# Kernel optimization log

Measured on AMD Instinct MI355X. Metric: run time of the kernel, lower is better.

Reference implementation:

```python
import jax, jax.numpy as jnp
import numpy as np


def _conv1x1(x, W, b):
    # x: [b,c,h,w], W: [out,in], b: [out]
    return jnp.einsum('oi,bihw->bohw', W, x) + b[None, :, None, None]


def setup_inputs() -> dict:
    key = jax.random.key(0)
    ks = jax.random.split(key, 8)
    B, C, H, W = 4, 256, 64, 64
    s = 1.0 / np.sqrt(C)
    return {
        'x1': jax.random.normal(ks[0], (B, C, H, W), jnp.float32),
        'x2': jax.random.normal(ks[1], (B, C, H, W), jnp.float32),
        'Wq': jax.random.normal(ks[2], (C, C), jnp.float32) * s,
        'bq': jax.random.normal(ks[3], (C,), jnp.float32) * 0.01,
        'Wk': jax.random.normal(ks[4], (C, C), jnp.float32) * s,
        'bk': jax.random.normal(ks[5], (C,), jnp.float32) * 0.01,
        'Wv': jax.random.normal(ks[6], (C, C), jnp.float32) * s,
        'bv': jax.random.normal(ks[7], (C,), jnp.float32) * 0.01,
    }


def reference(x1, x2, Wq, bq, Wk, bk, Wv, bv):
    b, c, h, w = x1.shape
    n = h * w
    q = _conv1x1(x1, Wq, bq).reshape(b, c, n)   # [b,c,n]
    k = _conv1x1(x2, Wk, bk).reshape(b, c, n)   # [b,c,n]
    v = _conv1x1(x2, Wv, bv).reshape(b, c, n)   # [b,c,n]
    # scores[b,i,j] = sum_c q[b,c,i] * k[b,c,j]; softmax over j (last dim)
    scores = jnp.einsum('bci,bcj->bij', q, k)
    attn = jax.nn.softmax(scores, axis=-1)      # [b,n,n]
    # out[b,c,i] = sum_j v[b,c,j] * attn[b,i,j]  (v @ attn^T)
    out = jnp.einsum('bcj,bij->bci', v, attn)
    return out.reshape(b, c, h, w)
```

## Files before the change

### kernel.cpp

```cpp
#include <hip/hip_runtime.h>

#define BATCH 4
#define CDIM 256
#define NDIM 4096

typedef unsigned short u16;
typedef unsigned int u32;
typedef _Float16 f16;
typedef __attribute__((ext_vector_type(8))) _Float16 half8;
typedef __attribute__((ext_vector_type(4))) float floatx4;

__device__ __forceinline__ void load_lds_128(const void* g, void* l) {
  __builtin_amdgcn_global_load_lds(
      (const __attribute__((address_space(1))) u32*)g,
      (__attribute__((address_space(3))) u32*)l, 16, 0, 0);
}

__global__ __launch_bounds__(256) void prep_w_k(
    const float* __restrict__ wq, const float* __restrict__ wk,
    const float* __restrict__ wv, f16* __restrict__ whq,
    f16* __restrict__ whk, f16* __restrict__ whv) {
  const int gid = blockIdx.x * 256 + threadIdx.x;
  const int a = gid >> 13;
  const int r = gid & 8191;
  const float* src = (a == 0) ? wq : ((a == 1) ? wk : wv);
  f16* dst = (a == 0) ? whq : ((a == 1) ? whk : whv);
  float4 v0 = *(const float4*)(src + r * 8);
  float4 v1 = *(const float4*)(src + r * 8 + 4);
  half8 h;
  h[0] = (f16)v0.x; h[1] = (f16)v0.y; h[2] = (f16)v0.z; h[3] = (f16)v0.w;
  h[4] = (f16)v1.x; h[5] = (f16)v1.y; h[6] = (f16)v1.z; h[7] = (f16)v1.w;
  *(half8*)(dst + r * 8) = h;
}

__global__ __launch_bounds__(256) void transpose_k(
    const float* __restrict__ x1, const float* __restrict__ x2,
    f16* __restrict__ xt1, f16* __restrict__ xt2) {
  __shared__ __align__(16) float tile[64 * 68];
  const int z = blockIdx.z;
  const float* src = (z & 1) ? x2 : x1;
  f16* dst = (z & 1) ? xt2 : xt1;
  const int b = z >> 1;
  src += (size_t)b * CDIM * NDIM;
  dst += (size_t)b * NDIM * CDIM;
  const int n0 = blockIdx.x * 64, c0 = blockIdx.y * 64;
  const int t = threadIdx.x;
#pragma unroll
  for (int it = 0; it < 4; ++it) {
    int chunk = t + it * 256;
    int row = chunk >> 4;
    int col4 = (chunk & 15) << 2;
    float4 v = *(const float4*)(src + (size_t)(c0 + row) * NDIM + (n0 + col4));
    *(float4*)&tile[row * 68 + col4] = v;
  }
  __syncthreads();
#pragma unroll
  for (int it = 0; it < 2; ++it) {
    int task = t + it * 256;
    int nl = task >> 3;
    int cb = (task & 7) << 3;
    half8 h;
#pragma unroll
    for (int j = 0; j < 8; ++j) h[j] = (f16)tile[(cb + j) * 68 + nl];
    *(half8*)(dst + (size_t)(n0 + nl) * CDIM + (c0 + cb)) = h;
  }
}

__global__ __launch_bounds__(256, 2) void proj_qk_k(
    const f16* __restrict__ xt1, const f16* __restrict__ xt2,
    const f16* __restrict__ whq, const float* __restrict__ bq,
    const f16* __restrict__ whk, const float* __restrict__ bk,
    f16* __restrict__ qt, f16* __restrict__ kt) {
  const int z = blockIdx.z;
  const int which = z & 1, b = z >> 1;
  const f16* xt = which ? xt2 : xt1;
  const f16* w = which ? whk : whq;
  const float* bias = which ? bk : bq;
  f16* outp = which ? kt : qt;
  xt += (size_t)b * NDIM * CDIM;
  outp += (size_t)b * NDIM * CDIM;
  const int c0 = blockIdx.x * 128, i0 = blockIdx.y * 128;
  const int tid = threadIdx.x;
  const int wave = tid >> 6, lane = tid & 63, l16 = lane & 15, grp = lane >> 4;
  const int wi = (wave & 1) * 64, wc = (wave >> 1) * 64;
  floatx4 acc[4][4];
#pragma unroll
  for (int mb = 0; mb < 4; ++mb)
#pragma unroll
    for (int nb = 0; nb < 4; ++nb) acc[mb][nb] = (floatx4){0.f, 0.f, 0.f, 0.f};
#pragma unroll
  for (int ks = 0; ks < 8; ++ks) {
    const int kofs = ks * 32 + grp * 8;
    half8 a[4], bb[4];
#pragma unroll
    for (int mb = 0; mb < 4; ++mb)
      a[mb] = *(const half8*)(xt + (size_t)(i0 + wi + mb * 16 + l16) * CDIM + kofs);
#pragma unroll
    for (int nb = 0; nb < 4; ++nb)
      bb[nb] = *(const half8*)(w + (size_t)(c0 + wc + nb * 16 + l16) * CDIM + kofs);
#pragma unroll
    for (int mb = 0; mb < 4; ++mb)
#pragma unroll
      for (int nb = 0; nb < 4; ++nb)
        acc[mb][nb] = __builtin_amdgcn_mfma_f32_16x16x32_f16(a[mb], bb[nb], acc[mb][nb], 0, 0, 0);
  }
#pragma unroll
  for (int nb = 0; nb < 4; ++nb) {
    const int c = c0 + wc + nb * 16 + l16;
    const float bv = bias[c];
#pragma unroll
    for (int mb = 0; mb < 4; ++mb) {
      const int ibase = i0 + wi + mb * 16 + grp * 4;
#pragma unroll
      for (int r = 0; r < 4; ++r)
        outp[(size_t)(ibase + r) * CDIM + c] = (f16)(acc[mb][nb][r] + bv);
    }
  }
}

__global__ __launch_bounds__(256, 2) void proj_v_k(
    const f16* __restrict__ xt2, const f16* __restrict__ whv,
    const float* __restrict__ bv, f16* __restrict__ vsout) {
  const int b = blockIdx.z;
  const f16* xt = xt2 + (size_t)b * NDIM * CDIM;
  f16* outp = vsout + (size_t)b * CDIM * NDIM;
  const int c0 = blockIdx.x * 128, j0 = blockIdx.y * 128;
  const int tid = threadIdx.x;
  const int wave = tid >> 6, lane = tid & 63, l16 = lane & 15, grp = lane >> 4;
  const int wc = (wave & 1) * 64, wj = (wave >> 1) * 64;
  floatx4 acc[4][4];
#pragma unroll
  for (int mb = 0; mb < 4; ++mb)
#pragma unroll
    for (int nb = 0; nb < 4; ++nb) acc[mb][nb] = (floatx4){0.f, 0.f, 0.f, 0.f};
#pragma unroll
  for (int ks = 0; ks < 8; ++ks) {
    const int kofs = ks * 32 + grp * 8;
    half8 a[4], bb[4];
#pragma unroll
    for (int mb = 0; mb < 4; ++mb)
      a[mb] = *(const half8*)(whv + (size_t)(c0 + wc + mb * 16 + l16) * CDIM + kofs);
#pragma unroll
    for (int nb = 0; nb < 4; ++nb)
      bb[nb] = *(const half8*)(xt + (size_t)(j0 + wj + nb * 16 + l16) * CDIM + kofs);
#pragma unroll
    for (int mb = 0; mb < 4; ++mb)
#pragma unroll
      for (int nb = 0; nb < 4; ++nb)
        acc[mb][nb] = __builtin_amdgcn_mfma_f32_16x16x32_f16(a[mb], bb[nb], acc[mb][nb], 0, 0, 0);
  }
#pragma unroll
  for (int mb = 0; mb < 4; ++mb)
#pragma unroll
    for (int r = 0; r < 4; ++r) {
      const int c = c0 + wc + mb * 16 + grp * 4 + r;
      const float bvv = bv[c];
#pragma unroll
      for (int nb = 0; nb < 4; ++nb) {
        const int j = j0 + wj + nb * 16 + l16;
        outp[(size_t)c * NDIM + j] = (f16)(acc[mb][nb][r] + bvv);
      }
    }
}

__global__ __launch_bounds__(256) void flash_k(
    const f16* __restrict__ qt, const f16* __restrict__ kt,
    const f16* __restrict__ vs, float* __restrict__ outp) {
  __shared__ __align__(16) u16 smem[2 * 32768 + 4096];
  const int bx = blockIdx.x;
  const int b = (bx & 7) >> 1;
  const int i0 = ((bx >> 3) + ((bx & 1) << 5)) * 64;
  const f16* Q = qt + (size_t)b * NDIM * CDIM;
  const f16* K = kt + (size_t)b * NDIM * CDIM;
  const f16* V = vs + (size_t)b * CDIM * NDIM;
  float* outg = outp + (size_t)b * CDIM * NDIM;
  const int tid = threadIdx.x;
  const int wave = tid >> 6, lane = tid & 63, l16 = lane & 15, grp = lane >> 4;

  half8 qf[8];
#pragma unroll
  for (int ks = 0; ks < 8; ++ks)
    qf[ks] = *(const half8*)(Q + (size_t)(i0 + wave * 16 + l16) * CDIM + ks * 32 + grp * 8);

  floatx4 O[16];
#pragma unroll
  for (int cb = 0; cb < 16; ++cb) O[cb] = (floatx4){0.f, 0.f, 0.f, 0.f};
  float mrow[4], lrow[4];
#pragma unroll
  for (int r = 0; r < 4; ++r) { mrow[r] = -1e30f; lrow[r] = 0.f; }

  f16* sPh = (f16*)(smem + 65536);
  f16* sPw = sPh + wave * (16 * 64);

  const int kr2 = lane >> 5, kp = lane & 31;
  const int vr = lane >> 3, vp = lane & 7;

#define STAGE(J0, BUF)                                                        \
  {                                                                           \
    u16* bK = (BUF);                                                          \
    u16* bV = (BUF) + 16384;                                                  \
    _Pragma("unroll") for (int it = 0; it < 8; ++it) {                        \
      const int row = wave * 16 + it * 2 + kr2;                               \
      const int g = kp ^ (row & 7);                                           \
      load_lds_128(K + (size_t)((J0) + row) * CDIM + g * 8,                   \
                   &bK[(wave * 16 + it * 2) * 256]);                          \
    }                                                                         \
    _Pragma("unroll") for (int it = 0; it < 8; ++it) {                        \
      const int c = wave * 64 + it * 8 + vr;                                  \
      const int g = vp ^ (c & 7);                                             \
      load_lds_128(V + (size_t)c * NDIM + (J0) + g * 8,                       \
                   &bV[(wave * 64 + it * 8) * 64]);                           \
    }                                                                         \
  }

  STAGE(0, smem)

  for (int t = 0; t < NDIM / 64; ++t) {
    __syncthreads();
    if (t + 1 < NDIM / 64) STAGE((t + 1) * 64, smem + ((t + 1) & 1) * 32768)
    u16* bK = smem + (t & 1) * 32768;
    u16* bV = bK + 16384;

    floatx4 S4[4];
#pragma unroll
    for (int jb = 0; jb < 4; ++jb) S4[jb] = (floatx4){0.f, 0.f, 0.f, 0.f};
#pragma unroll
    for (int ks = 0; ks < 8; ++ks) {
      const int chunk = ks * 4 + grp;
#pragma unroll
      for (int jb = 0; jb < 4; ++jb) {
        const int row = jb * 16 + l16;
        half8 kf = *(const half8*)&bK[row * 256 + ((chunk ^ (row & 7)) << 3)];
        S4[jb] = __builtin_amdgcn_mfma_f32_16x16x32_f16(qf[ks], kf, S4[jb], 0, 0, 0);
      }
    }

    float mnew[4];
#pragma unroll
    for (int r = 0; r < 4; ++r)
      mnew[r] = fmaxf(fmaxf(S4[0][r], S4[1][r]), fmaxf(S4[2][r], S4[3][r]));
#pragma unroll
    for (int mask = 1; mask < 16; mask <<= 1)
#pragma unroll
      for (int r = 0; r < 4; ++r)
        mnew[r] = fmaxf(mnew[r], __shfl_xor(mnew[r], mask, 64));
    float alpha[4];
#pragma unroll
    for (int r = 0; r < 4; ++r) {
      const float mt = fmaxf(mrow[r], mnew[r]);
      alpha[r] = __expf(mrow[r] - mt);
      mrow[r] = mt;
    }
    float rsum[4];
#pragma unroll
    for (int r = 0; r < 4; ++r) {
#pragma unroll
      for (int jb = 0; jb < 4; ++jb) S4[jb][r] = __expf(S4[jb][r] - mrow[r]);
      rsum[r] = (S4[0][r] + S4[1][r]) + (S4[2][r] + S4[3][r]);
    }
#pragma unroll
    for (int mask = 1; mask < 16; mask <<= 1)
#pragma unroll
      for (int r = 0; r < 4; ++r)
        rsum[r] += __shfl_xor(rsum[r], mask, 64);
#pragma unroll
    for (int r = 0; r < 4; ++r) lrow[r] = lrow[r] * alpha[r] + rsum[r];
#pragma unroll
    for (int cb = 0; cb < 16; ++cb)
#pragma unroll
      for (int r = 0; r < 4; ++r) O[cb][r] *= alpha[r];

#pragma unroll
    for (int jb = 0; jb < 4; ++jb)
#pragma unroll
      for (int r = 0; r < 4; ++r) {
        const int row = grp * 4 + r;
        const int col = jb * 16 + l16;
        sPw[row * 64 + (((col >> 3) ^ (row & 7)) << 3) + (col & 7)] = (f16)S4[jb][r];
      }
    half8 pa[2];
#pragma unroll
    for (int ks = 0; ks < 2; ++ks) {
      const int chunk = ks * 4 + grp;
      pa[ks] = *(const half8*)&sPw[l16 * 64 + ((chunk ^ (l16 & 7)) << 3)];
    }

#pragma unroll
    for (int ks = 0; ks < 2; ++ks) {
      const int chunk = ks * 4 + grp;
#pragma unroll
      for (int cb = 0; cb < 16; ++cb) {
        const int c = cb * 16 + l16;
        half8 vf = *(const half8*)&bV[c * 64 + ((chunk ^ (c & 7)) << 3)];
        O[cb] = __builtin_amdgcn_mfma_f32_16x16x32_f16(pa[ks], vf, O[cb], 0, 0, 0);
      }
    }
  }
  __syncthreads();

  float inv[4];
#pragma unroll
  for (int r = 0; r < 4; ++r) inv[r] = 1.0f / lrow[r];
  float* sO = (float*)smem;
#pragma unroll
  for (int cb = 0; cb < 16; ++cb) {
    const int c = cb * 16 + l16;
#pragma unroll
    for (int r = 0; r < 4; ++r)
      sO[c * 68 + wave * 16 + grp * 4 + r] = O[cb][r] * inv[r];
  }
  __syncthreads();
#pragma unroll
  for (int it = 0; it < 16; ++it) {
    const int idx = tid + it * 256;
    const int c = idx >> 4, p = idx & 15;
    float4 v = *(const float4*)&sO[c * 68 + p * 4];
    *(float4*)(outg + (size_t)c * NDIM + i0 + p * 4) = v;
  }
}

extern "C" void kernel_launch(void* const* d_in, const int* in_sizes, int n_in,
                              void* d_out, int out_size, void* d_ws, size_t ws_size,
                              hipStream_t stream) {
  const float* x1 = (const float*)d_in[0];
  const float* x2 = (const float*)d_in[1];
  const float* Wq = (const float*)d_in[2];
  const float* bq = (const float*)d_in[3];
  const float* Wk = (const float*)d_in[4];
  const float* bk = (const float*)d_in[5];
  const float* Wv = (const float*)d_in[6];
  const float* bv = (const float*)d_in[7];
  float* out = (float*)d_out;
  char* ws = (char*)d_ws;
  const size_t SZ = (size_t)BATCH * NDIM * CDIM * sizeof(f16);
  f16* xt1 = (f16*)(ws + 0 * SZ);
  f16* xt2 = (f16*)(ws + 1 * SZ);
  f16* qt  = (f16*)(ws + 2 * SZ);
  f16* kt  = (f16*)(ws + 3 * SZ);
  f16* vsp = (f16*)(ws + 4 * SZ);
  f16* whq = (f16*)(ws + 5 * SZ);
  f16* whk = whq + CDIM * CDIM;
  f16* whv = whk + CDIM * CDIM;

  prep_w_k<<<dim3(96), dim3(256), 0, stream>>>(Wq, Wk, Wv, whq, whk, whv);
  transpose_k<<<dim3(NDIM / 64, CDIM / 64, 2 * BATCH), dim3(256), 0, stream>>>(x1, x2, xt1, xt2);
  proj_qk_k<<<dim3(2, 32, 2 * BATCH), dim3(256), 0, stream>>>(xt1, xt2, whq, bq, whk, bk, qt, kt);
  proj_v_k<<<dim3(2, 32, BATCH), dim3(256), 0, stream>>>(xt2, whv, bv, vsp);
  flash_k<<<dim3(256), dim3(256), 0, stream>>>(qt, kt, vsp, out);
}
```

Before: 290.5 us.

## Split flash attention over key dimension with partial outputs and combine kernel

```diff
diff --git a/kernel.cpp b/kernel.cpp
--- a/kernel.cpp
+++ b/kernel.cpp
@@ -3,6 +3,10 @@
 #define BATCH 4
 #define CDIM 256
 #define NDIM 4096
+#define SPLITS 4
+#define KSPLIT (NDIM / SPLITS)
+#define JT 64
+#define NTILES (KSPLIT / JT)
 
 typedef unsigned short u16;
 typedef unsigned int u32;
@@ -163,67 +167,68 @@
     }
 }
 
-__global__ __launch_bounds__(256) void flash_k(
+__global__ __launch_bounds__(256, 2) void flash_k(
     const f16* __restrict__ qt, const f16* __restrict__ kt,
-    const f16* __restrict__ vs, float* __restrict__ outp) {
-  __shared__ __align__(16) u16 smem[2 * 32768 + 4096];
+    const f16* __restrict__ vs, f16* __restrict__ pO,
+    float* __restrict__ pm, float* __restrict__ pl) {
+  __shared__ __align__(16) u16 smem[32768];
   const int bx = blockIdx.x;
-  const int b = (bx & 7) >> 1;
-  const int i0 = ((bx >> 3) + ((bx & 1) << 5)) * 64;
+  const int c16 = bx & 15;
+  const int b = c16 >> 2, s = c16 & 3;
+  const int i0 = (bx >> 4) * 128;
+  const int jwin = s * KSPLIT;
   const f16* Q = qt + (size_t)b * NDIM * CDIM;
   const f16* K = kt + (size_t)b * NDIM * CDIM;
   const f16* V = vs + (size_t)b * CDIM * NDIM;
-  float* outg = outp + (size_t)b * CDIM * NDIM;
   const int tid = threadIdx.x;
   const int wave = tid >> 6, lane = tid & 63, l16 = lane & 15, grp = lane >> 4;
-
-  half8 qf[8];
-#pragma unroll
-  for (int ks = 0; ks < 8; ++ks)
-    qf[ks] = *(const half8*)(Q + (size_t)(i0 + wave * 16 + l16) * CDIM + ks * 32 + grp * 8);
-
-  floatx4 O[16];
-#pragma unroll
-  for (int cb = 0; cb < 16; ++cb) O[cb] = (floatx4){0.f, 0.f, 0.f, 0.f};
-  float mrow[4], lrow[4];
-#pragma unroll
-  for (int r = 0; r < 4; ++r) { mrow[r] = -1e30f; lrow[r] = 0.f; }
-
-  f16* sPh = (f16*)(smem + 65536);
-  f16* sPw = sPh + wave * (16 * 64);
+  u16* bK = smem;
+  u16* bV = smem + 16384;
+
+  half8 qf[2][8];
+#pragma unroll
+  for (int mb = 0; mb < 2; ++mb)
+#pragma unroll
+    for (int ks = 0; ks < 8; ++ks)
+      qf[mb][ks] = *(const half8*)(Q + (size_t)(i0 + wave * 32 + mb * 16 + l16) * CDIM +
+                                   ks * 32 + grp * 8);
+
+  floatx4 O[2][16];
+#pragma unroll
+  for (int mb = 0; mb < 2; ++mb)
+#pragma unroll
+    for (int cb = 0; cb < 16; ++cb) O[mb][cb] = (floatx4){0.f, 0.f, 0.f, 0.f};
+  float m_[2][4], l_[2][4];
+#pragma unroll
+  for (int mb = 0; mb < 2; ++mb)
+#pragma unroll
+    for (int r = 0; r < 4; ++r) { m_[mb][r] = -1e30f; l_[mb][r] = 0.f; }
 
   const int kr2 = lane >> 5, kp = lane & 31;
   const int vr = lane >> 3, vp = lane & 7;
 
-#define STAGE(J0, BUF)                                                        \
-  {                                                                           \
-    u16* bK = (BUF);                                                          \
-    u16* bV = (BUF) + 16384;                                                  \
-    _Pragma("unroll") for (int it = 0; it < 8; ++it) {                        \
-      const int row = wave * 16 + it * 2 + kr2;                               \
-      const int g = kp ^ (row & 7);                                           \
-      load_lds_128(K + (size_t)((J0) + row) * CDIM + g * 8,                   \
-                   &bK[(wave * 16 + it * 2) * 256]);                          \
-    }                                                                         \
-    _Pragma("unroll") for (int it = 0; it < 8; ++it) {                        \
-      const int c = wave * 64 + it * 8 + vr;                                  \
-      const int g = vp ^ (c & 7);                                             \
-      load_lds_128(V + (size_t)c * NDIM + (J0) + g * 8,                       \
-                   &bV[(wave * 64 + it * 8) * 64]);                           \
-    }                                                                         \
-  }
-
-  STAGE(0, smem)
-
-  for (int t = 0; t < NDIM / 64; ++t) {
+  for (int tt = 0; tt < NTILES; ++tt) {
+    const int j0 = jwin + tt * JT;
     __syncthreads();
-    if (t + 1 < NDIM / 64) STAGE((t + 1) * 64, smem + ((t + 1) & 1) * 32768)
-    u16* bK = smem + (t & 1) * 32768;
-    u16* bV = bK + 16384;
-
-    floatx4 S4[4];
-#pragma unroll
-    for (int jb = 0; jb < 4; ++jb) S4[jb] = (floatx4){0.f, 0.f, 0.f, 0.f};
+#pragma unroll
+    for (int it = 0; it < 8; ++it) {
+      const int row = wave * 16 + it * 2 + kr2;
+      const int g = kp ^ (row & 7);
+      load_lds_128(K + (size_t)(j0 + row) * CDIM + g * 8, &bK[(wave * 16 + it * 2) * 256]);
+    }
+#pragma unroll
+    for (int it = 0; it < 8; ++it) {
+      const int c = wave * 64 + it * 8 + vr;
+      const int g = vp ^ (c & 7);
+      load_lds_128(V + (size_t)c * NDIM + j0 + g * 8, &bV[(wave * 64 + it * 8) * 64]);
+    }
+    __syncthreads();
+
+    floatx4 S[2][4];
+#pragma unroll
+    for (int mb = 0; mb < 2; ++mb)
+#pragma unroll
+      for (int jb = 0; jb < 4; ++jb) S[mb][jb] = (floatx4){0.f, 0.f, 0.f, 0.f};
 #pragma unroll
     for (int ks = 0; ks < 8; ++ks) {
       const int chunk = ks * 4 + grp;
@@ -231,58 +236,65 @@
       for (int jb = 0; jb < 4; ++jb) {
         const int row = jb * 16 + l16;
         half8 kf = *(const half8*)&bK[row * 256 + ((chunk ^ (row & 7)) << 3)];
-        S4[jb] = __builtin_amdgcn_mfma_f32_16x16x32_f16(qf[ks], kf, S4[jb], 0, 0, 0);
-      }
-    }
-
-    float mnew[4];
-#pragma unroll
-    for (int r = 0; r < 4; ++r)
-      mnew[r] = fmaxf(fmaxf(S4[0][r], S4[1][r]), fmaxf(S4[2][r], S4[3][r]));
-#pragma unroll
-    for (int mask = 1; mask < 16; mask <<= 1)
+        S[0][jb] = __builtin_amdgcn_mfma_f32_16x16x32_f16(qf[0][ks], kf, S[0][jb], 0, 0, 0);
+        S[1][jb] = __builtin_amdgcn_mfma_f32_16x16x32_f16(qf[1][ks], kf, S[1][jb], 0, 0, 0);
+      }
+    }
+
+#pragma unroll
+    for (int mb = 0; mb < 2; ++mb) {
+      float mnew[4];
 #pragma unroll
       for (int r = 0; r < 4; ++r)
-        mnew[r] = fmaxf(mnew[r], __shfl_xor(mnew[r], mask, 64));
-    float alpha[4];
-#pragma unroll
-    for (int r = 0; r < 4; ++r) {
-      const float mt = fmaxf(mrow[r], mnew[r]);
-      alpha[r] = __expf(mrow[r] - mt);
-      mrow[r] = mt;
-    }
-    float rsum[4];
-#pragma unroll
-    for (int r = 0; r < 4; ++r) {
-#pragma unroll
-      for (int jb = 0; jb < 4; ++jb) S4[jb][r] = __expf(S4[jb][r] - mrow[r]);
-      rsum[r] = (S4[0][r] + S4[1][r]) + (S4[2][r] + S4[3][r]);
-    }
-#pragma unroll
-    for (int mask = 1; mask < 16; mask <<= 1)
-#pragma unroll
-      for (int r = 0; r < 4; ++r)
-        rsum[r] += __shfl_xor(rsum[r], mask, 64);
-#pragma unroll
-    for (int r = 0; r < 4; ++r) lrow[r] = lrow[r] * alpha[r] + rsum[r];
-#pragma unroll
-    for (int cb = 0; cb < 16; ++cb)
-#pragma unroll
-      for (int r = 0; r < 4; ++r) O[cb][r] *= alpha[r];
-
-#pragma unroll
-    for (int jb = 0; jb < 4; ++jb)
+        mnew[r] = fmaxf(fmaxf(S[mb][0][r], S[mb][1][r]), fmaxf(S[mb][2][r], S[mb][3][r]));
+#pragma unroll
+      for (int mask = 1; mask < 16; mask <<= 1)
+#pragma unroll
+        for (int r = 0; r < 4; ++r) mnew[r] = fmaxf(mnew[r], __shfl_xor(mnew[r], mask, 64));
+      float alpha[4], rs[4];
 #pragma unroll
       for (int r = 0; r < 4; ++r) {
-        const int row = grp * 4 + r;
-        const int col = jb * 16 + l16;
-        sPw[row * 64 + (((col >> 3) ^ (row & 7)) << 3) + (col & 7)] = (f16)S4[jb][r];
-      }
-    half8 pa[2];
-#pragma unroll
-    for (int ks = 0; ks < 2; ++ks) {
-      const int chunk = ks * 4 + grp;
-      pa[ks] = *(const half8*)&sPw[l16 * 64 + ((chunk ^ (l16 & 7)) << 3)];
+        const float mt = fmaxf(m_[mb][r], mnew[r]);
+        alpha[r] = __expf(m_[mb][r] - mt);
+        m_[mb][r] = mt;
+      }
+#pragma unroll
+      for (int r = 0; r < 4; ++r) {
+#pragma unroll
+        for (int jb = 0; jb < 4; ++jb) S[mb][jb][r] = __expf(S[mb][jb][r] - m_[mb][r]);
+        rs[r] = (S[mb][0][r] + S[mb][1][r]) + (S[mb][2][r] + S[mb][3][r]);
+      }
+#pragma unroll
+      for (int mask = 1; mask < 16; mask <<= 1)
+#pragma unroll
+        for (int r = 0; r < 4; ++r) rs[r] += __shfl_xor(rs[r], mask, 64);
+#pragma unroll
+      for (int r = 0; r < 4; ++r) l_[mb][r] = l_[mb][r] * alpha[r] + rs[r];
+#pragma unroll
+      for (int cb = 0; cb < 16; ++cb)
+#pragma unroll
+        for (int r = 0; r < 4; ++r) O[mb][cb][r] *= alpha[r];
+    }
+    __syncthreads();
+
+    float* Pw = (float*)smem + wave * 1088;
+    half8 pa[2][2];
+#pragma unroll
+    for (int mb = 0; mb < 2; ++mb) {
+#pragma unroll
+      for (int jb = 0; jb < 4; ++jb)
+#pragma unroll
+        for (int r = 0; r < 4; ++r)
+          Pw[(grp * 4 + r) * 68 + jb * 16 + l16] = S[mb][jb][r];
+#pragma unroll
+      for (int ks = 0; ks < 2; ++ks) {
+        floatx4 u0 = *(const floatx4*)&Pw[l16 * 68 + ks * 32 + grp * 8];
+        floatx4 u1 = *(const floatx4*)&Pw[l16 * 68 + ks * 32 + grp * 8 + 4];
+        half8 h;
+        h[0] = (f16)u0[0]; h[1] = (f16)u0[1]; h[2] = (f16)u0[2]; h[3] = (f16)u0[3];
+        h[4] = (f16)u1[0]; h[5] = (f16)u1[1]; h[6] = (f16)u1[2]; h[7] = (f16)u1[3];
+        pa[mb][ks] = h;
+      }
     }
 
 #pragma unroll
@@ -292,30 +304,96 @@
       for (int cb = 0; cb < 16; ++cb) {
         const int c = cb * 16 + l16;
         half8 vf = *(const half8*)&bV[c * 64 + ((chunk ^ (c & 7)) << 3)];
-        O[cb] = __builtin_amdgcn_mfma_f32_16x16x32_f16(pa[ks], vf, O[cb], 0, 0, 0);
-      }
-    }
+        O[0][cb] = __builtin_amdgcn_mfma_f32_16x16x32_f16(pa[0][ks], vf, O[0][cb], 0, 0, 0);
+        O[1][cb] = __builtin_amdgcn_mfma_f32_16x16x32_f16(pa[1][ks], vf, O[1][cb], 0, 0, 0);
+      }
+    }
+  }
+
+#pragma unroll
+  for (int quarter = 0; quarter < 4; ++quarter) {
+    __syncthreads();
+    float* sO = (float*)smem;
+#pragma unroll
+    for (int mb = 0; mb < 2; ++mb)
+#pragma unroll
+      for (int cb4 = 0; cb4 < 4; ++cb4) {
+        const int cb = quarter * 4 + cb4;
+        const int cl = cb4 * 16 + l16;
+        const int i = wave * 32 + mb * 16 + grp * 4;
+        *(floatx4*)&sO[cl * 132 + i] = O[mb][cb];
+      }
+    __syncthreads();
+    const size_t obase = ((size_t)(b * SPLITS + s) * CDIM + quarter * 64) * NDIM + i0;
+#pragma unroll
+    for (int it = 0; it < 4; ++it) {
+      const int task = tid + it * 256;
+      const int cl = task >> 4, p = (task & 15) * 8;
+      floatx4 v0 = *(const floatx4*)&sO[cl * 132 + p];
+      floatx4 v1 = *(const floatx4*)&sO[cl * 132 + p + 4];
+      half8 h;
+      h[0] = (f16)v0[0]; h[1] = (f16)v0[1]; h[2] = (f16)v0[2]; h[3] = (f16)v0[3];
+      h[4] = (f16)v1[0]; h[5] = (f16)v1[1]; h[6] = (f16)v1[2]; h[7] = (f16)v1[3];
+      *(half8*)(pO + obase + (size_t)cl * NDIM + p) = h;
+    }
+  }
+  if (l16 == 0) {
+    const int base = (b * SPLITS + s) * NDIM + i0;
+#pragma unroll
+    for (int mb = 0; mb < 2; ++mb)
+#pragma unroll
+      for (int r = 0; r < 4; ++r) {
+        const int i = wave * 32 + mb * 16 + grp * 4 + r;
+        pm[base + i] = m_[mb][r];
+        pl[base + i] = l_[mb][r];
+      }
+  }
+}
+
+__global__ __launch_bounds__(256) void combine_k(
+    const f16* __restrict__ pO, const float* __restrict__ pm,
+    const float* __restrict__ pl, float* __restrict__ out) {
+  __shared__ float su[SPLITS][64];
+  const int b = blockIdx.x >> 6;
+  const int i0 = (blockIdx.x & 63) * 64;
+  const int t = threadIdx.x;
+  if (t < 64) {
+    const int i = i0 + t;
+    float mv[SPLITS], w[SPLITS];
+    float M = -3e38f;
+#pragma unroll
+    for (int s = 0; s < SPLITS; ++s) {
+      mv[s] = pm[(b * SPLITS + s) * NDIM + i];
+      M = fmaxf(M, mv[s]);
+    }
+    float L = 0.f;
+#pragma unroll
+    for (int s = 0; s < SPLITS; ++s) {
+      w[s] = __expf(mv[s] - M);
+      L += pl[(b * SPLITS + s) * NDIM + i] * w[s];
+    }
+    const float invL = 1.0f / L;
+#pragma unroll
+    for (int s = 0; s < SPLITS; ++s) su[s][t] = w[s] * invL;
   }
   __syncthreads();
-
-  float inv[4];
-#pragma unroll
-  for (int r = 0; r < 4; ++r) inv[r] = 1.0f / lrow[r];
-  float* sO = (float*)smem;
-#pragma unroll
-  for (int cb = 0; cb < 16; ++cb) {
-    const int c = cb * 16 + l16;
-#pragma unroll
-    for (int r = 0; r < 4; ++r)
-      sO[c * 68 + wave * 16 + grp * 4 + r] = O[cb][r] * inv[r];
-  }
-  __syncthreads();
-#pragma unroll
-  for (int it = 0; it < 16; ++it) {
-    const int idx = tid + it * 256;
-    const int c = idx >> 4, p = idx & 15;
-    float4 v = *(const float4*)&sO[c * 68 + p * 4];
-    *(float4*)(outg + (size_t)c * NDIM + i0 + p * 4) = v;
+#pragma unroll
+  for (int it = 0; it < 8; ++it) {
+    const int task = t + it * 256;
+    const int c = task >> 3, p = (task & 7) * 8;
+    float acc[8] = {0.f, 0.f, 0.f, 0.f, 0.f, 0.f, 0.f, 0.f};
+#pragma unroll
+    for (int s = 0; s < SPLITS; ++s) {
+      const f16* src = pO + ((size_t)(b * SPLITS + s) * CDIM + c) * NDIM + i0 + p;
+      half8 h = *(const half8*)src;
+#pragma unroll
+      for (int j = 0; j < 8; ++j) acc[j] += su[s][p + j] * (float)h[j];
+    }
+    float* dst = out + ((size_t)b * CDIM + c) * NDIM + i0 + p;
+    float4 lo = {acc[0], acc[1], acc[2], acc[3]};
+    float4 hi = {acc[4], acc[5], acc[6], acc[7]};
+    *(float4*)dst = lo;
+    *(float4*)(dst + 4) = hi;
   }
 }
 
@@ -332,19 +410,22 @@
   const float* bv = (const float*)d_in[7];
   float* out = (float*)d_out;
   char* ws = (char*)d_ws;
-  const size_t SZ = (size_t)BATCH * NDIM * CDIM * sizeof(f16);
-  f16* xt1 = (f16*)(ws + 0 * SZ);
-  f16* xt2 = (f16*)(ws + 1 * SZ);
-  f16* qt  = (f16*)(ws + 2 * SZ);
-  f16* kt  = (f16*)(ws + 3 * SZ);
-  f16* vsp = (f16*)(ws + 4 * SZ);
-  f16* whq = (f16*)(ws + 5 * SZ);
+  f16* qtp = (f16*)(ws + 0);
+  f16* ktp = (f16*)(ws + 8388608);
+  f16* vsp = (f16*)(ws + 16777216);
+  f16* xt1 = (f16*)(ws + 25165824);
+  f16* xt2 = (f16*)(ws + 33554432);
+  f16* whq = (f16*)(ws + 41943040);
   f16* whk = whq + CDIM * CDIM;
   f16* whv = whk + CDIM * CDIM;
+  f16* pO = (f16*)(ws + 25165824);
+  float* pm = (float*)(ws + 58720256);
+  float* pl = (float*)(ws + 58982400);
 
   prep_w_k<<<dim3(96), dim3(256), 0, stream>>>(Wq, Wk, Wv, whq, whk, whv);
   transpose_k<<<dim3(NDIM / 64, CDIM / 64, 2 * BATCH), dim3(256), 0, stream>>>(x1, x2, xt1, xt2);
-  proj_qk_k<<<dim3(2, 32, 2 * BATCH), dim3(256), 0, stream>>>(xt1, xt2, whq, bq, whk, bk, qt, kt);
+  proj_qk_k<<<dim3(2, 32, 2 * BATCH), dim3(256), 0, stream>>>(xt1, xt2, whq, bq, whk, bk, qtp, ktp);
   proj_v_k<<<dim3(2, 32, BATCH), dim3(256), 0, stream>>>(xt2, whv, bv, vsp);
-  flash_k<<<dim3(256), dim3(256), 0, stream>>>(qt, kt, vsp, out);
-}
+  flash_k<<<dim3(512), dim3(256), 0, stream>>>(qtp, ktp, vsp, pO, pm, pl);
+  combine_k<<<dim3(256), dim3(256), 0, stream>>>(pO, pm, pl, out);
+}
```

After: 395.3 us. 1.36x slower.
